# Kernel tuning notes

Hardware: AMD Instinct MI355X
Metric: run time of the kernel (lower is better)

The kernel has to match this reference:

```python
import jax, jax.numpy as jnp
import numpy as np

B, T, N, C, H = 8, 96, 1024, 64, 64  # batch, in_len, nodes, hidden_dim, MLP hidden
NUM_TYPES, EMB = 3, 8
GROUPS = 4


def setup_inputs() -> dict:
    key = jax.random.key(0)
    ks = jax.random.split(key, 16)
    s = 0.05
    return {
        "x": jax.random.normal(ks[0], (B, T, 1, N), jnp.float32),
        "adj": jax.random.uniform(ks[1], (N, N), jnp.float32) / N,  # row-normalized-ish
        "node_type": jax.random.randint(ks[2], (N,), 0, NUM_TYPES),
        # input_projection: Conv1d(1, C, 1) -> per-channel scale + bias
        "w_in": jax.random.normal(ks[3], (C,), jnp.float32) * np.sqrt(2.0),
        "b_in": jnp.zeros((C,), jnp.float32),
        # GCN params
        "weights_pool": jax.random.normal(ks[4], (EMB, C, C), jnp.float32) * np.sqrt(2.0 / (EMB + C)),
        "node_emb": jax.random.normal(ks[5], (NUM_TYPES, EMB), jnp.float32) * s,
        # GroupNorm(4, C)
        "gn_w": jnp.ones((C,), jnp.float32),
        "gn_b": jnp.zeros((C,), jnp.float32),
        # ResBlock temporal MLP: Linear(T,H) then Linear(H,T)
        "w1": jax.random.normal(ks[6], (H, T), jnp.float32) * np.sqrt(1.0 / T),
        "b1": jnp.zeros((H,), jnp.float32),
        "w2": jax.random.normal(ks[7], (T, H), jnp.float32) * np.sqrt(1.0 / H),
        "b2": jnp.zeros((T,), jnp.float32),
        # out_projection: Conv1d(C, 1, 1)
        "w_out": jax.random.normal(ks[8], (C,), jnp.float32) * np.sqrt(2.0 / C),
        "b_out": jnp.zeros((), jnp.float32),
    }


def reference(x, adj, node_type, w_in, b_in, weights_pool, node_emb,
              gn_w, gn_b, w1, b1, w2, b2, w_out, b_out):
    Bx, Tx, _, Nx = x.shape
    BT = Bx * Tx
    # input_projection: Conv1d(1->C, k=1) on (BT, 1, N)
    h = x.reshape(BT, Nx)                                   # channel dim is 1
    h = h[:, None, :] * w_in[None, :, None] + b_in[None, :, None]   # (BT, C, N)
    x_in = h
    # --- GCN with adaptive per-node weights ---
    feats = jnp.swapaxes(h, 1, 2)                            # (BT, N, C)
    nt_emb = node_emb[node_type]                             # gather -> (N, 8)
    node_w = jnp.einsum('nd,dio->nio', nt_emb, weights_pool) # (N, C, C)
    feats = jnp.einsum('nm,bmi->bni', adj, feats)            # adj @ feats
    feats = jnp.einsum('bni,nio->bno', feats, node_w)        # per-node matmul
    h = jnp.swapaxes(feats, 1, 2) + x_in                     # (BT, C, N)
    # --- GroupNorm(4, C), eps=1e-5 ---
    g = h.reshape(BT, GROUPS, C // GROUPS, Nx)
    mu = g.mean(axis=(2, 3), keepdims=True)
    var = g.var(axis=(2, 3), keepdims=True)
    g = (g - mu) / jnp.sqrt(var + 1e-5)
    h = g.reshape(BT, C, Nx) * gn_w[None, :, None] + gn_b[None, :, None]
    # --- temporal mixer: (b t) c n -> (b n) t c ---
    h = h.reshape(Bx, Tx, C, Nx).transpose(0, 3, 1, 2).reshape(Bx * Nx, Tx, C)
    ht = jnp.swapaxes(h, 1, 2)                               # (BN, C, T)
    t = jax.nn.relu(ht @ w1.T + b1) @ w2.T + b2              # (BN, C, T)
    h = h + jnp.swapaxes(t, 1, 2)                            # (BN, T, C)
    # --- silu + out_projection: Conv1d(C->1, k=1) over (BN, C, T) ---
    y = jax.nn.silu(jnp.swapaxes(h, 1, 2))                   # (BN, C, T)
    y = jnp.einsum('bct,c->bt', y, w_out) + b_out            # (BN, T)
    y = y.reshape(Bx, Nx, Tx).transpose(0, 2, 1)[:, :, None, :]  # (B, T, 1, N)
    return y
```

## Files before the change

### kernel.cpp

```cpp
#include <hip/hip_runtime.h>
#include <hip/hip_bf16.h>
#include <math.h>

#define B_   8
#define T_   96
#define N_   1024
#define C_   64
#define H_   64
#define BT_  768
#define EMB_ 8

typedef __attribute__((ext_vector_type(8))) short short8v;
typedef __attribute__((ext_vector_type(4))) float f32x4;

__device__ __forceinline__ ushort f2bf(float f) {
    unsigned int u = __float_as_uint(f);
    unsigned int r = (u + 0x7fffu + ((u >> 16) & 1u)) >> 16;
    return (ushort)r;
}
__device__ __forceinline__ float bf2f(ushort h) {
    return __uint_as_float(((unsigned int)h) << 16);
}

__global__ __launch_bounds__(256) void k_setup(const float* __restrict__ wpool,
                                               const float* __restrict__ w_in,
                                               const float* __restrict__ b_in,
                                               const float* __restrict__ emb,
                                               const float* __restrict__ w1,
                                               const float* __restrict__ w2,
                                               const float* __restrict__ x,
                                               ushort* __restrict__ wfrag1,
                                               ushort* __restrict__ wfrag2,
                                               float* __restrict__ xT,
                                               float* __restrict__ WT,
                                               float* __restrict__ BTb,
                                               float* __restrict__ TAB,
                                               float* __restrict__ GG) {
    int bid = blockIdx.x;
    int tid = threadIdx.x;
    if (bid == 0) {
        for (int e = tid; e < 6144; e += 256) {
            int j = e & 7, lane = (e >> 3) & 63, frag = e >> 9;
            int mt = frag / 3, k0 = frag - 3 * mt;
            int h = 16 * mt + (lane & 15);
            int t = 32 * k0 + 8 * (lane >> 4) + j;
            wfrag1[e] = f2bf(w1[h * T_ + t]);
        }
    } else if (bid == 1) {
        for (int e = tid; e < 6144; e += 256) {
            int j = e & 7, lane = (e >> 3) & 63, frag = e >> 9;
            int mt2 = frag >> 1, ks = frag & 1;
            int t = 16 * mt2 + (lane & 15);
            int h = 32 * ks + 8 * (lane >> 4) + j;
            wfrag2[e] = f2bf(w2[t * H_ + h]);
        }
    } else if (bid < 194) {
        __shared__ float tile[64][65];
        int tnum = bid - 2;
        int ti = tnum >> 4;
        int tj = tnum & 15;
#pragma unroll
        for (int k = 0; k < 16; ++k) {
            int idx = tid + 256 * k;
            int r = idx >> 6, cq = idx & 63;
            tile[r][cq] = x[(ti * 64 + r) * N_ + tj * 64 + cq];
        }
        __syncthreads();
#pragma unroll
        for (int k = 0; k < 16; ++k) {
            int idx = tid + 256 * k;
            int r = idx >> 6, cq = idx & 63;
            xT[(tj * 64 + r) * BT_ + ti * 64 + cq] = tile[cq][r];
        }
    } else {
        __shared__ float wp1s[512], wpbs[512];
        for (int e = tid; e < 512; e += 256) {
            int d = e >> 6, cc = e & 63;
            float s1 = 0.f, s2 = 0.f;
            for (int i = 0; i < 64; ++i) {
                float w = wpool[(d * 64 + i) * 64 + cc];
                s1 += w_in[i] * w;
                s2 += b_in[i] * w;
            }
            wp1s[e] = s1;
            wpbs[e] = s2;
        }
        __syncthreads();
        int wave = tid >> 6, lane = tid & 63;
        int lq = lane & 15, g = lane >> 4;
        if (wave < 3) {
            int ty = wave, cc = lane;
            float w = 0.f, bb = 0.f;
#pragma unroll
            for (int d = 0; d < EMB_; ++d) {
                float ev = emb[ty * EMB_ + d];
                w += ev * wp1s[d * C_ + cc];
                bb += ev * wpbs[d * C_ + cc];
            }
            WT[ty * C_ + cc] = w;
            BTb[ty * C_ + cc] = bb;
            float wi = w_in[cc], bi = b_in[cc];
            float vals[9] = {w, bb, w * w, bb * bb, w * wi, w * bi, wi * bb, bb * bi, w * bb};
#pragma unroll
            for (int q = 0; q < 9; ++q) {
                vals[q] += __shfl_xor(vals[q], 1);
                vals[q] += __shfl_xor(vals[q], 2);
                vals[q] += __shfl_xor(vals[q], 4);
                vals[q] += __shfl_xor(vals[q], 8);
            }
            if (lq == 0) {
#pragma unroll
                for (int q = 0; q < 9; ++q) TAB[(ty * 4 + g) * 9 + q] = vals[q];
            }
        } else {
            int cc = lane;
            float wi = w_in[cc], bi = b_in[cc];
            float v5[5] = {wi, bi, wi * wi, bi * bi, wi * bi};
#pragma unroll
            for (int q = 0; q < 5; ++q) {
                v5[q] += __shfl_xor(v5[q], 1);
                v5[q] += __shfl_xor(v5[q], 2);
                v5[q] += __shfl_xor(v5[q], 4);
                v5[q] += __shfl_xor(v5[q], 8);
            }
            if (lq == 0) {
#pragma unroll
                for (int q = 0; q < 5; ++q) GG[g * 5 + q] = v5[q];
            }
        }
    }
}

__global__ __launch_bounds__(256, 4) void k_ax(const float* __restrict__ x,
                                               const float* __restrict__ adj,
                                               float* __restrict__ axo,
                                               float* __restrict__ axT,
                                               float* __restrict__ rs) {
    __shared__ ushort Xs[32 * 64];
    __shared__ ushort As[32 * 64];
    const int tid = threadIdx.x;
    const int wave = tid >> 6, lane = tid & 63;
    const int lq = lane & 15, g4 = lane >> 4;
    const int n0 = blockIdx.x * 32, m0 = blockIdx.y * 32;
    const int mi = wave >> 1, ni = wave & 1;
    const int sr = tid >> 3, sq = tid & 7;
    const int sqx = sq ^ (sr & 7);
    const int ra = 16 * mi + lq, rb = 16 * ni + lq;

    f32x4 acc = {0.f, 0.f, 0.f, 0.f};
    float rsacc = 0.f;

    for (int k0 = 0; k0 < N_; k0 += 64) {
        __syncthreads();
        {
            const float* px = x + (m0 + sr) * N_ + k0 + sq * 8;
            float4 xa = *(const float4*)px;
            float4 xb = *(const float4*)(px + 4);
            union { short8v v; __hip_bfloat162 h[4]; } o;
            o.h[0] = __float22bfloat162_rn(make_float2(xa.x, xa.y));
            o.h[1] = __float22bfloat162_rn(make_float2(xa.z, xa.w));
            o.h[2] = __float22bfloat162_rn(make_float2(xb.x, xb.y));
            o.h[3] = __float22bfloat162_rn(make_float2(xb.z, xb.w));
            *(short8v*)&Xs[sr * 64 + sqx * 8] = o.v;

            const float* pa = adj + (n0 + sr) * N_ + k0 + sq * 8;
            float4 aa = *(const float4*)pa;
            float4 ab = *(const float4*)(pa + 4);
            if (m0 == 0)
                rsacc += aa.x + aa.y + aa.z + aa.w + ab.x + ab.y + ab.z + ab.w;
            o.h[0] = __float22bfloat162_rn(make_float2(aa.x, aa.y));
            o.h[1] = __float22bfloat162_rn(make_float2(aa.z, aa.w));
            o.h[2] = __float22bfloat162_rn(make_float2(ab.x, ab.y));
            o.h[3] = __float22bfloat162_rn(make_float2(ab.z, ab.w));
            *(short8v*)&As[sr * 64 + sqx * 8] = o.v;
        }
        __syncthreads();
#pragma unroll
        for (int ks = 0; ks < 2; ++ks) {
            short8v a = *(const short8v*)&Xs[ra * 64 + ((4 * ks + g4) ^ (ra & 7)) * 8];
            short8v bb = *(const short8v*)&As[rb * 64 + ((4 * ks + g4) ^ (rb & 7)) * 8];
            acc = __builtin_amdgcn_mfma_f32_16x16x32_bf16(a, bb, acc, 0, 0, 0);
        }
    }
    if (m0 == 0) {
        rsacc += __shfl_xor(rsacc, 1);
        rsacc += __shfl_xor(rsacc, 2);
        rsacc += __shfl_xor(rsacc, 4);
        if (sq == 0) rs[n0 + sr] = rsacc;
    }
#pragma unroll
    for (int r = 0; r < 4; ++r)
        axo[(m0 + 16 * mi + 4 * g4 + r) * N_ + n0 + 16 * ni + lq] = acc[r];
    float4 tv = make_float4(acc[0], acc[1], acc[2], acc[3]);
    *(float4*)&axT[(n0 + 16 * ni + lq) * BT_ + m0 + 16 * mi + 4 * g4] = tv;
}

__global__ __launch_bounds__(256) void k_gn(const float* __restrict__ x,
                                            const float* __restrict__ ax,
                                            const float* __restrict__ rs,
                                            const int* __restrict__ ntype,
                                            const float* __restrict__ TAB,
                                            const float* __restrict__ GG,
                                            float* __restrict__ muT,
                                            float* __restrict__ rgT) {
    int bt = blockIdx.x;
    int tid = threadIdx.x;
    const float* axr = ax + bt * N_;
    const float* xr = x + bt * N_;
    float S[23];
#pragma unroll
    for (int q = 0; q < 23; ++q) S[q] = 0.f;
#pragma unroll
    for (int i = 0; i < 4; ++i) {
        int n = tid + 256 * i;
        float a = axr[n], xv = xr[n], r = rs[n];
        int ty = ntype[n];
        float e0 = (ty == 0) ? 1.f : 0.f;
        float e1 = (ty == 1) ? 1.f : 0.f;
        float e2 = (ty == 2) ? 1.f : 0.f;
        float a2 = a * a, axp = a * xv, ar = a * r, xrr = xv * r, r2 = r * r;
        S[0] += e0 * a;   S[1] += e1 * a;   S[2] += e2 * a;
        S[3] += e0 * r;   S[4] += e1 * r;   S[5] += e2 * r;
        S[6] += e0 * a2;  S[7] += e1 * a2;  S[8] += e2 * a2;
        S[9] += e0 * r2;  S[10] += e1 * r2; S[11] += e2 * r2;
        S[12] += e0 * axp; S[13] += e1 * axp; S[14] += e2 * axp;
        S[15] += e0 * ar; S[16] += e1 * ar; S[17] += e2 * ar;
        S[18] += e0 * xrr; S[19] += e1 * xrr; S[20] += e2 * xrr;
        S[21] += xv;      S[22] += xv * xv;
    }
#pragma unroll
    for (int q = 0; q < 23; ++q) {
#pragma unroll
        for (int off = 32; off; off >>= 1) S[q] += __shfl_down(S[q], off);
    }
    __shared__ float wred[4][23];
    __shared__ float tot[23];
    int wave = tid >> 6, lane = tid & 63;
    if (lane == 0) {
#pragma unroll
        for (int q = 0; q < 23; ++q) wred[wave][q] = S[q];
    }
    __syncthreads();
    if (tid < 23) tot[tid] = wred[0][tid] + wred[1][tid] + wred[2][tid] + wred[3][tid];
    __syncthreads();
    if (tid < 4) {
        int g = tid;
        float M = 0.f, Q = 0.f;
#pragma unroll
        for (int ty = 0; ty < 3; ++ty) {
            const float* tb = TAB + (ty * 4 + g) * 9;
            float A1v = tot[0 + ty], R1v = tot[3 + ty], A2v = tot[6 + ty];
            float R2v = tot[9 + ty], AXv = tot[12 + ty], ARv = tot[15 + ty];
            float XRv = tot[18 + ty];
            M += tb[0] * A1v + tb[1] * R1v;
            Q += tb[2] * A2v + tb[3] * R2v +
                 2.f * (tb[4] * AXv + tb[5] * A1v + tb[6] * XRv + tb[7] * R1v + tb[8] * ARv);
        }
        float Sx = tot[21], Sx2 = tot[22];
        const float* gg = GG + g * 5;
        M += gg[0] * Sx + 1024.f * gg[1];
        Q += gg[2] * Sx2 + 2.f * gg[4] * Sx + 1024.f * gg[3];
        const float inv = 1.f / 16384.f;
        float m = M * inv;
        float v = Q * inv - m * m;
        int b = bt / T_, t = bt - b * T_;
        muT[(b * 4 + g) * T_ + t] = m;
        rgT[(b * 4 + g) * T_ + t] = rsqrtf(v + 1e-5f);
    }
}

__global__ __launch_bounds__(256, 4) void k_main(const float* __restrict__ xT,
                                                 const float* __restrict__ axT,
                                                 const float* __restrict__ rs,
                                                 const int* __restrict__ ntype,
                                                 const float* __restrict__ WT,
                                                 const float* __restrict__ BTb,
                                                 const float* __restrict__ muT,
                                                 const float* __restrict__ rgT,
                                                 const float* __restrict__ w_in,
                                                 const float* __restrict__ b_in,
                                                 const float* __restrict__ gn_w,
                                                 const float* __restrict__ gn_b,
                                                 const ushort* __restrict__ wfrag1,
                                                 const ushort* __restrict__ wfrag2,
                                                 const float* __restrict__ b1,
                                                 const float* __restrict__ b2,
                                                 const float* __restrict__ w_out,
                                                 const float* __restrict__ b_out,
                                                 float* __restrict__ out) {
    __shared__ ushort Hs[64 * 104];
    __shared__ ushort Hd[64 * 104];
    __shared__ float axs[4][96], xs[4][96];
    __shared__ float musT[4 * 100], rgsT[4 * 100];
    __shared__ float redp[4][96][4];

    const int tid = threadIdx.x;
    const int n0 = blockIdx.x * 4;
    const int b = blockIdx.y;
    const int wm = tid >> 6;
    const int lane = tid & 63;
    const int lq = lane & 15;
    const int g4 = lane >> 4;

    short8v w1f[4][3];
#pragma unroll
    for (int mt = 0; mt < 4; ++mt)
#pragma unroll
        for (int k0 = 0; k0 < 3; ++k0)
            w1f[mt][k0] = *(const short8v*)(wfrag1 + (((mt * 3 + k0) << 6) + lane) * 8);

    for (int j = tid; j < 384; j += 256) {
        int nn = j / 96, t = j - nn * 96;
        axs[nn][t] = axT[(n0 + nn) * BT_ + b * T_ + t];
        xs[nn][t] = xT[(n0 + nn) * BT_ + b * T_ + t];
    }
    for (int j = tid; j < 384; j += 256) {
        int g = j / 96, t = j - 96 * g;
        musT[g * 100 + t] = muT[b * 384 + j];
        rgsT[g * 100 + t] = rgT[b * 384 + j];
    }

    const int c = 16 * wm + lq;
    const float wic = w_in[c], bic = b_in[c];
    const float gwc = gn_w[c], gbc = gn_b[c];

    const int4 ty4 = *(const int4*)&ntype[n0];
    const float4 rs4 = *(const float4*)&rs[n0];
    float wlc4[4], base4[4];
    {
        const float wlcA[3] = {WT[c], WT[64 + c], WT[128 + c]};
        const float blcA[3] = {BTb[c], BTb[64 + c], BTb[128 + c]};
        const int tys[4] = {ty4.x, ty4.y, ty4.z, ty4.w};
        const float rss[4] = {rs4.x, rs4.y, rs4.z, rs4.w};
#pragma unroll
        for (int nn = 0; nn < 4; ++nn) {
            int ty = tys[nn];
            float wlc = (ty == 0) ? wlcA[0] : (ty == 1) ? wlcA[1] : wlcA[2];
            float blc = (ty == 0) ? blcA[0] : (ty == 1) ? blcA[1] : blcA[2];
            wlc4[nn] = wlc;
            base4[nn] = rss[nn] * blc + bic;
        }
    }
    __syncthreads();

    const ushort* wf2p = wfrag2;
    const float* b1p = b1;
    const float* b2p = b2;
    const float* wop = w_out;

#pragma unroll 1
    for (int nn = 0; nn < 4; ++nn) {
        asm volatile("" : "+s"(wf2p), "+s"(b1p), "+s"(b2p), "+s"(wop));
        const float wlc = wlc4[nn];
        const float base = base4[nn];

        f32x4 acc1[4] = {{0.f, 0.f, 0.f, 0.f}, {0.f, 0.f, 0.f, 0.f},
                         {0.f, 0.f, 0.f, 0.f}, {0.f, 0.f, 0.f, 0.f}};
#pragma unroll
        for (int k0 = 0; k0 < 3; ++k0) {
            int t8 = 32 * k0 + 8 * g4;
            float4 a0 = *(const float4*)&axs[nn][t8];
            float4 a1 = *(const float4*)&axs[nn][t8 + 4];
            float4 x0 = *(const float4*)&xs[nn][t8];
            float4 x1 = *(const float4*)&xs[nn][t8 + 4];
            float4 m0 = *(const float4*)&musT[wm * 100 + t8];
            float4 m1 = *(const float4*)&musT[wm * 100 + t8 + 4];
            float4 r0 = *(const float4*)&rgsT[wm * 100 + t8];
            float4 r1 = *(const float4*)&rgsT[wm * 100 + t8 + 4];
            float vv[8];
            vv[0] = ((a0.x * wlc + x0.x * wic + base) - m0.x) * (r0.x * gwc) + gbc;
            vv[1] = ((a0.y * wlc + x0.y * wic + base) - m0.y) * (r0.y * gwc) + gbc;
            vv[2] = ((a0.z * wlc + x0.z * wic + base) - m0.z) * (r0.z * gwc) + gbc;
            vv[3] = ((a0.w * wlc + x0.w * wic + base) - m0.w) * (r0.w * gwc) + gbc;
            vv[4] = ((a1.x * wlc + x1.x * wic + base) - m1.x) * (r1.x * gwc) + gbc;
            vv[5] = ((a1.y * wlc + x1.y * wic + base) - m1.y) * (r1.y * gwc) + gbc;
            vv[6] = ((a1.z * wlc + x1.z * wic + base) - m1.z) * (r1.z * gwc) + gbc;
            vv[7] = ((a1.w * wlc + x1.w * wic + base) - m1.w) * (r1.w * gwc) + gbc;
            union { short8v v; __hip_bfloat162 h2[4]; } o;
            o.h2[0] = __float22bfloat162_rn(make_float2(vv[0], vv[1]));
            o.h2[1] = __float22bfloat162_rn(make_float2(vv[2], vv[3]));
            o.h2[2] = __float22bfloat162_rn(make_float2(vv[4], vv[5]));
            o.h2[3] = __float22bfloat162_rn(make_float2(vv[6], vv[7]));
            *(short8v*)&Hs[c * 104 + t8] = o.v;
#pragma unroll
            for (int mt = 0; mt < 4; ++mt)
                acc1[mt] = __builtin_amdgcn_mfma_f32_16x16x32_bf16(w1f[mt][k0], o.v, acc1[mt], 0, 0, 0);
        }

#pragma unroll
        for (int mt = 0; mt < 4; ++mt) {
            float4 b1v = *(const float4*)(b1p + 16 * mt + 4 * g4);
            __hip_bfloat162 p0 = __float22bfloat162_rn(make_float2(
                fmaxf(acc1[mt][0] + b1v.x, 0.f), fmaxf(acc1[mt][1] + b1v.y, 0.f)));
            __hip_bfloat162 p1 = __float22bfloat162_rn(make_float2(
                fmaxf(acc1[mt][2] + b1v.z, 0.f), fmaxf(acc1[mt][3] + b1v.w, 0.f)));
            union { uint2 u; __hip_bfloat162 h2[2]; } w;
            w.h2[0] = p0; w.h2[1] = p1;
            *(uint2*)&Hd[c * 104 + 16 * mt + 4 * g4] = w.u;
        }

        f32x4 acc2[6] = {{0.f, 0.f, 0.f, 0.f}, {0.f, 0.f, 0.f, 0.f},
                         {0.f, 0.f, 0.f, 0.f}, {0.f, 0.f, 0.f, 0.f},
                         {0.f, 0.f, 0.f, 0.f}, {0.f, 0.f, 0.f, 0.f}};
#pragma unroll
        for (int ks = 0; ks < 2; ++ks) {
            short8v af = *(const short8v*)&Hd[c * 104 + 32 * ks + 8 * g4];
#pragma unroll
            for (int mt2 = 0; mt2 < 6; ++mt2) {
                short8v bf = *(const short8v*)(wf2p + (((mt2 * 2 + ks) << 6) + lane) * 8);
                acc2[mt2] = __builtin_amdgcn_mfma_f32_16x16x32_bf16(af, bf, acc2[mt2], 0, 0, 0);
            }
        }

        float4 wo4 = *(const float4*)(wop + 16 * wm + 4 * g4);
#pragma unroll
        for (int mt2 = 0; mt2 < 6; ++mt2) {
            int tv = 16 * mt2 + lq;
            float bz = b2p[tv];
            float pm = 0.f;
#pragma unroll
            for (int r = 0; r < 4; ++r) {
                float res = bf2f(Hs[(16 * wm + 4 * g4 + r) * 104 + tv]);
                float z = res + acc2[mt2][r] + bz;
                float sg = __builtin_amdgcn_rcpf(1.f + __expf(-z));
                pm += z * sg * wo4[r];
            }
            pm += __shfl_xor(pm, 16);
            pm += __shfl_xor(pm, 32);
            if (g4 == 0) redp[nn][tv][wm] = pm;
        }
    }
    __syncthreads();

    if (tid < 96) {
        float bo = b_out[0];
        float4 y;
        float* py = (float*)&y;
#pragma unroll
        for (int nn = 0; nn < 4; ++nn) {
            float4 v = *(const float4*)&redp[nn][tid][0];
            py[nn] = v.x + v.y + v.z + v.w + bo;
        }
        *(float4*)&out[(b * T_ + tid) * N_ + n0] = y;
    }
}

extern "C" void kernel_launch(void* const* d_in, const int* in_sizes, int n_in,
                              void* d_out, int out_size, void* d_ws, size_t ws_size,
                              hipStream_t stream) {
    const float* x     = (const float*)d_in[0];
    const float* adj   = (const float*)d_in[1];
    const int*   ntype = (const int*)d_in[2];
    const float* w_in  = (const float*)d_in[3];
    const float* b_in  = (const float*)d_in[4];
    const float* wpool = (const float*)d_in[5];
    const float* emb   = (const float*)d_in[6];
    const float* gn_w  = (const float*)d_in[7];
    const float* gn_b  = (const float*)d_in[8];
    const float* w1    = (const float*)d_in[9];
    const float* b1    = (const float*)d_in[10];
    const float* w2    = (const float*)d_in[11];
    const float* b2    = (const float*)d_in[12];
    const float* w_out = (const float*)d_in[13];
    const float* b_out = (const float*)d_in[14];
    float* out = (float*)d_out;
    float* ws = (float*)d_ws;

    float* rsv  = ws + 1024;
    float* WT   = ws + 2048;
    float* BTb  = ws + 2240;
    float* TAB  = ws + 2432;
    float* GG   = ws + 2540;
    float* muT  = ws + 2560;
    float* rgT  = ws + 5632;
    ushort* wfrag1 = (ushort*)(ws + 8704);
    ushort* wfrag2 = (ushort*)(ws + 11776);
    float* axb  = ws + 14848;
    float* axTb = ws + 14848 + 786432;
    float* xTb  = ws + 14848 + 2 * 786432;

    k_setup<<<dim3(195), dim3(256), 0, stream>>>(wpool, w_in, b_in, emb, w1, w2, x,
                                                 wfrag1, wfrag2, xTb, WT, BTb, TAB, GG);
    k_ax<<<dim3(32, 24), dim3(256), 0, stream>>>(x, adj, axb, axTb, rsv);
    k_gn<<<dim3(768), dim3(256), 0, stream>>>(x, axb, rsv, ntype, TAB, GG, muT, rgT);
    k_main<<<dim3(256, 8), dim3(256), 0, stream>>>(xTb, axTb, rsv, ntype, WT, BTb,
                                                   muT, rgT, w_in, b_in, gn_w, gn_b,
                                                   wfrag1, wfrag2, b1, b2,
                                                   w_out, b_out, out);
}
```

Before: 83.21 us.

## Merge setup and adj-matmul kernels; precompute GroupNorm affine in registers in main

The setup kernel and the adj@x MFMA kernel are merged into one launch with a block-id dispatch and a shared-memory union. This removes one kernel launch and lets the two independent workloads run concurrently. In k_main, the shared-memory staging of mu and rstd is replaced by per-thread register loads folded with gn_w and gn_b into FMA form. The w1 fragments are now reloaded from global memory inside the loop instead of held in registers, trading register pressure for extra loads.

Result: no change. 83.47 us (+0.3%).

```diff
diff --git a/kernel.cpp b/kernel.cpp
--- a/kernel.cpp
+++ b/kernel.cpp
@@ -22,23 +22,88 @@
     return __uint_as_float(((unsigned int)h) << 16);
 }
 
-__global__ __launch_bounds__(256) void k_setup(const float* __restrict__ wpool,
-                                               const float* __restrict__ w_in,
-                                               const float* __restrict__ b_in,
-                                               const float* __restrict__ emb,
-                                               const float* __restrict__ w1,
-                                               const float* __restrict__ w2,
-                                               const float* __restrict__ x,
-                                               ushort* __restrict__ wfrag1,
-                                               ushort* __restrict__ wfrag2,
-                                               float* __restrict__ xT,
-                                               float* __restrict__ WT,
-                                               float* __restrict__ BTb,
-                                               float* __restrict__ TAB,
-                                               float* __restrict__ GG) {
-    int bid = blockIdx.x;
-    int tid = threadIdx.x;
-    if (bid == 0) {
+__global__ __launch_bounds__(256, 4) void k_pre(const float* __restrict__ x,
+                                                const float* __restrict__ adj,
+                                                const float* __restrict__ wpool,
+                                                const float* __restrict__ w_in,
+                                                const float* __restrict__ b_in,
+                                                const float* __restrict__ emb,
+                                                const float* __restrict__ w1,
+                                                const float* __restrict__ w2,
+                                                float* __restrict__ axo,
+                                                float* __restrict__ axT,
+                                                float* __restrict__ rs,
+                                                ushort* __restrict__ wfrag1,
+                                                ushort* __restrict__ wfrag2,
+                                                float* __restrict__ xT,
+                                                float* __restrict__ WT,
+                                                float* __restrict__ BTb,
+                                                float* __restrict__ TAB,
+                                                float* __restrict__ GG) {
+    __shared__ union UU {
+        struct { ushort Xs[32 * 64]; ushort As[32 * 64]; } g;
+        float tile[64][65];
+        struct { float wp1s[512]; float wpbs[512]; } tab;
+    } U;
+    const int bid = blockIdx.x;
+    const int tid = threadIdx.x;
+
+    if (bid < 768) {
+        const int wave = tid >> 6, lane = tid & 63;
+        const int lq = lane & 15, g4 = lane >> 4;
+        const int n0 = (bid & 31) * 32, m0 = (bid >> 5) * 32;
+        const int mi = wave >> 1, ni = wave & 1;
+        const int sr = tid >> 3, sq = tid & 7;
+        const int sqx = sq ^ (sr & 7);
+        const int ra = 16 * mi + lq, rb = 16 * ni + lq;
+
+        f32x4 acc = {0.f, 0.f, 0.f, 0.f};
+        float rsacc = 0.f;
+
+        for (int k0 = 0; k0 < N_; k0 += 64) {
+            __syncthreads();
+            {
+                const float* px = x + (m0 + sr) * N_ + k0 + sq * 8;
+                float4 xa = *(const float4*)px;
+                float4 xb = *(const float4*)(px + 4);
+                union { short8v v; __hip_bfloat162 h[4]; } o;
+                o.h[0] = __float22bfloat162_rn(make_float2(xa.x, xa.y));
+                o.h[1] = __float22bfloat162_rn(make_float2(xa.z, xa.w));
+                o.h[2] = __float22bfloat162_rn(make_float2(xb.x, xb.y));
+                o.h[3] = __float22bfloat162_rn(make_float2(xb.z, xb.w));
+                *(short8v*)&U.g.Xs[sr * 64 + sqx * 8] = o.v;
+
+                const float* pa = adj + (n0 + sr) * N_ + k0 + sq * 8;
+                float4 aa = *(const float4*)pa;
+                float4 ab = *(const float4*)(pa + 4);
+                if (m0 == 0)
+                    rsacc += aa.x + aa.y + aa.z + aa.w + ab.x + ab.y + ab.z + ab.w;
+                o.h[0] = __float22bfloat162_rn(make_float2(aa.x, aa.y));
+                o.h[1] = __float22bfloat162_rn(make_float2(aa.z, aa.w));
+                o.h[2] = __float22bfloat162_rn(make_float2(ab.x, ab.y));
+                o.h[3] = __float22bfloat162_rn(make_float2(ab.z, ab.w));
+                *(short8v*)&U.g.As[sr * 64 + sqx * 8] = o.v;
+            }
+            __syncthreads();
+#pragma unroll
+            for (int ks = 0; ks < 2; ++ks) {
+                short8v a = *(const short8v*)&U.g.Xs[ra * 64 + ((4 * ks + g4) ^ (ra & 7)) * 8];
+                short8v bb = *(const short8v*)&U.g.As[rb * 64 + ((4 * ks + g4) ^ (rb & 7)) * 8];
+                acc = __builtin_amdgcn_mfma_f32_16x16x32_bf16(a, bb, acc, 0, 0, 0);
+            }
+        }
+        if (m0 == 0) {
+            rsacc += __shfl_xor(rsacc, 1);
+            rsacc += __shfl_xor(rsacc, 2);
+            rsacc += __shfl_xor(rsacc, 4);
+            if (sq == 0) rs[n0 + sr] = rsacc;
+        }
+#pragma unroll
+        for (int r = 0; r < 4; ++r)
+            axo[(m0 + 16 * mi + 4 * g4 + r) * N_ + n0 + 16 * ni + lq] = acc[r];
+        float4 tv = make_float4(acc[0], acc[1], acc[2], acc[3]);
+        *(float4*)&axT[(n0 + 16 * ni + lq) * BT_ + m0 + 16 * mi + 4 * g4] = tv;
+    } else if (bid == 768) {
         for (int e = tid; e < 6144; e += 256) {
             int j = e & 7, lane = (e >> 3) & 63, frag = e >> 9;
             int mt = frag / 3, k0 = frag - 3 * mt;
@@ -46,7 +111,7 @@
             int t = 32 * k0 + 8 * (lane >> 4) + j;
             wfrag1[e] = f2bf(w1[h * T_ + t]);
         }
-    } else if (bid == 1) {
+    } else if (bid == 769) {
         for (int e = tid; e < 6144; e += 256) {
             int j = e & 7, lane = (e >> 3) & 63, frag = e >> 9;
             int mt2 = frag >> 1, ks = frag & 1;
@@ -54,26 +119,24 @@
             int h = 32 * ks + 8 * (lane >> 4) + j;
             wfrag2[e] = f2bf(w2[t * H_ + h]);
         }
-    } else if (bid < 194) {
-        __shared__ float tile[64][65];
-        int tnum = bid - 2;
+    } else if (bid < 962) {
+        int tnum = bid - 770;
         int ti = tnum >> 4;
         int tj = tnum & 15;
 #pragma unroll
         for (int k = 0; k < 16; ++k) {
             int idx = tid + 256 * k;
             int r = idx >> 6, cq = idx & 63;
-            tile[r][cq] = x[(ti * 64 + r) * N_ + tj * 64 + cq];
+            U.tile[r][cq] = x[(ti * 64 + r) * N_ + tj * 64 + cq];
         }
         __syncthreads();
 #pragma unroll
         for (int k = 0; k < 16; ++k) {
             int idx = tid + 256 * k;
             int r = idx >> 6, cq = idx & 63;
-            xT[(tj * 64 + r) * BT_ + ti * 64 + cq] = tile[cq][r];
+            xT[(tj * 64 + r) * BT_ + ti * 64 + cq] = U.tile[cq][r];
         }
     } else {
-        __shared__ float wp1s[512], wpbs[512];
         for (int e = tid; e < 512; e += 256) {
             int d = e >> 6, cc = e & 63;
             float s1 = 0.f, s2 = 0.f;
@@ -82,8 +145,8 @@
                 s1 += w_in[i] * w;
                 s2 += b_in[i] * w;
             }
-            wp1s[e] = s1;
-            wpbs[e] = s2;
+            U.tab.wp1s[e] = s1;
+            U.tab.wpbs[e] = s2;
         }
         __syncthreads();
         int wave = tid >> 6, lane = tid & 63;
@@ -94,8 +157,8 @@
 #pragma unroll
             for (int d = 0; d < EMB_; ++d) {
                 float ev = emb[ty * EMB_ + d];
-                w += ev * wp1s[d * C_ + cc];
-                bb += ev * wpbs[d * C_ + cc];
+                w += ev * U.tab.wp1s[d * C_ + cc];
+                bb += ev * U.tab.wpbs[d * C_ + cc];
             }
             WT[ty * C_ + cc] = w;
             BTb[ty * C_ + cc] = bb;
@@ -129,70 +192,6 @@
             }
         }
     }
-}
-
-__global__ __launch_bounds__(256, 4) void k_ax(const float* __restrict__ x,
-                                               const float* __restrict__ adj,
-                                               float* __restrict__ axo,
-                                               float* __restrict__ axT,
-                                               float* __restrict__ rs) {
-    __shared__ ushort Xs[32 * 64];
-    __shared__ ushort As[32 * 64];
-    const int tid = threadIdx.x;
-    const int wave = tid >> 6, lane = tid & 63;
-    const int lq = lane & 15, g4 = lane >> 4;
-    const int n0 = blockIdx.x * 32, m0 = blockIdx.y * 32;
-    const int mi = wave >> 1, ni = wave & 1;
-    const int sr = tid >> 3, sq = tid & 7;
-    const int sqx = sq ^ (sr & 7);
-    const int ra = 16 * mi + lq, rb = 16 * ni + lq;
-
-    f32x4 acc = {0.f, 0.f, 0.f, 0.f};
-    float rsacc = 0.f;
-
-    for (int k0 = 0; k0 < N_; k0 += 64) {
-        __syncthreads();
-        {
-            const float* px = x + (m0 + sr) * N_ + k0 + sq * 8;
-            float4 xa = *(const float4*)px;
-            float4 xb = *(const float4*)(px + 4);
-            union { short8v v; __hip_bfloat162 h[4]; } o;
-            o.h[0] = __float22bfloat162_rn(make_float2(xa.x, xa.y));
-            o.h[1] = __float22bfloat162_rn(make_float2(xa.z, xa.w));
-            o.h[2] = __float22bfloat162_rn(make_float2(xb.x, xb.y));
-            o.h[3] = __float22bfloat162_rn(make_float2(xb.z, xb.w));
-            *(short8v*)&Xs[sr * 64 + sqx * 8] = o.v;
-
-            const float* pa = adj + (n0 + sr) * N_ + k0 + sq * 8;
-            float4 aa = *(const float4*)pa;
-            float4 ab = *(const float4*)(pa + 4);
-            if (m0 == 0)
-                rsacc += aa.x + aa.y + aa.z + aa.w + ab.x + ab.y + ab.z + ab.w;
-            o.h[0] = __float22bfloat162_rn(make_float2(aa.x, aa.y));
-            o.h[1] = __float22bfloat162_rn(make_float2(aa.z, aa.w));
-            o.h[2] = __float22bfloat162_rn(make_float2(ab.x, ab.y));
-            o.h[3] = __float22bfloat162_rn(make_float2(ab.z, ab.w));
-            *(short8v*)&As[sr * 64 + sqx * 8] = o.v;
-        }
-        __syncthreads();
-#pragma unroll
-        for (int ks = 0; ks < 2; ++ks) {
-            short8v a = *(const short8v*)&Xs[ra * 64 + ((4 * ks + g4) ^ (ra & 7)) * 8];
-            short8v bb = *(const short8v*)&As[rb * 64 + ((4 * ks + g4) ^ (rb & 7)) * 8];
-            acc = __builtin_amdgcn_mfma_f32_16x16x32_bf16(a, bb, acc, 0, 0, 0);
-        }
-    }
-    if (m0 == 0) {
-        rsacc += __shfl_xor(rsacc, 1);
-        rsacc += __shfl_xor(rsacc, 2);
-        rsacc += __shfl_xor(rsacc, 4);
-        if (sq == 0) rs[n0 + sr] = rsacc;
-    }
-#pragma unroll
-    for (int r = 0; r < 4; ++r)
-        axo[(m0 + 16 * mi + 4 * g4 + r) * N_ + n0 + 16 * ni + lq] = acc[r];
-    float4 tv = make_float4(acc[0], acc[1], acc[2], acc[3]);
-    *(float4*)&axT[(n0 + 16 * ni + lq) * BT_ + m0 + 16 * mi + 4 * g4] = tv;
 }
 
 __global__ __launch_bounds__(256) void k_gn(const float* __restrict__ x,
@@ -291,7 +290,6 @@
     __shared__ ushort Hs[64 * 104];
     __shared__ ushort Hd[64 * 104];
     __shared__ float axs[4][96], xs[4][96];
-    __shared__ float musT[4 * 100], rgsT[4 * 100];
     __shared__ float redp[4][96][4];
 
     const int tid = threadIdx.x;
@@ -302,47 +300,37 @@
     const int lq = lane & 15;
     const int g4 = lane >> 4;
 
-    short8v w1f[4][3];
-#pragma unroll
-    for (int mt = 0; mt < 4; ++mt)
-#pragma unroll
-        for (int k0 = 0; k0 < 3; ++k0)
-            w1f[mt][k0] = *(const short8v*)(wfrag1 + (((mt * 3 + k0) << 6) + lane) * 8);
-
     for (int j = tid; j < 384; j += 256) {
         int nn = j / 96, t = j - nn * 96;
         axs[nn][t] = axT[(n0 + nn) * BT_ + b * T_ + t];
         xs[nn][t] = xT[(n0 + nn) * BT_ + b * T_ + t];
     }
-    for (int j = tid; j < 384; j += 256) {
-        int g = j / 96, t = j - 96 * g;
-        musT[g * 100 + t] = muT[b * 384 + j];
-        rgsT[g * 100 + t] = rgT[b * 384 + j];
-    }
 
     const int c = 16 * wm + lq;
     const float wic = w_in[c], bic = b_in[c];
     const float gwc = gn_w[c], gbc = gn_b[c];
-
-    const int4 ty4 = *(const int4*)&ntype[n0];
-    const float4 rs4 = *(const float4*)&rs[n0];
-    float wlc4[4], base4[4];
-    {
-        const float wlcA[3] = {WT[c], WT[64 + c], WT[128 + c]};
-        const float blcA[3] = {BTb[c], BTb[64 + c], BTb[128 + c]};
-        const int tys[4] = {ty4.x, ty4.y, ty4.z, ty4.w};
-        const float rss[4] = {rs4.x, rs4.y, rs4.z, rs4.w};
-#pragma unroll
-        for (int nn = 0; nn < 4; ++nn) {
-            int ty = tys[nn];
-            float wlc = (ty == 0) ? wlcA[0] : (ty == 1) ? wlcA[1] : wlcA[2];
-            float blc = (ty == 0) ? blcA[0] : (ty == 1) ? blcA[1] : blcA[2];
-            wlc4[nn] = wlc;
-            base4[nn] = rss[nn] * blc + bic;
-        }
+    const float wlcA[3] = {WT[c], WT[64 + c], WT[128 + c]};
+    const float blcA[3] = {BTb[c], BTb[64 + c], BTb[128 + c]};
+
+    float4 rgA[3], rgB[3], mgA[3], mgB[3];
+#pragma unroll
+    for (int k0 = 0; k0 < 3; ++k0) {
+        const float* mp = muT + b * 384 + wm * 96 + 32 * k0 + 8 * g4;
+        const float* rp = rgT + b * 384 + wm * 96 + 32 * k0 + 8 * g4;
+        float4 mA = *(const float4*)mp;
+        float4 mB = *(const float4*)(mp + 4);
+        float4 rA = *(const float4*)rp;
+        float4 rB = *(const float4*)(rp + 4);
+        rgA[k0] = make_float4(rA.x * gwc, rA.y * gwc, rA.z * gwc, rA.w * gwc);
+        rgB[k0] = make_float4(rB.x * gwc, rB.y * gwc, rB.z * gwc, rB.w * gwc);
+        mgA[k0] = make_float4(gbc - mA.x * rgA[k0].x, gbc - mA.y * rgA[k0].y,
+                              gbc - mA.z * rgA[k0].z, gbc - mA.w * rgA[k0].w);
+        mgB[k0] = make_float4(gbc - mB.x * rgB[k0].x, gbc - mB.y * rgB[k0].y,
+                              gbc - mB.z * rgB[k0].z, gbc - mB.w * rgB[k0].w);
     }
     __syncthreads();
 
+    const ushort* wf1p = wfrag1;
     const ushort* wf2p = wfrag2;
     const float* b1p = b1;
     const float* b2p = b2;
@@ -350,9 +338,12 @@
 
 #pragma unroll 1
     for (int nn = 0; nn < 4; ++nn) {
-        asm volatile("" : "+s"(wf2p), "+s"(b1p), "+s"(b2p), "+s"(wop));
-        const float wlc = wlc4[nn];
-        const float base = base4[nn];
+        asm volatile("" : "+s"(wf1p), "+s"(wf2p), "+s"(b1p), "+s"(b2p), "+s"(wop));
+        const int n = n0 + nn;
+        const int ty = ntype[n];
+        const float wlc = (ty == 0) ? wlcA[0] : (ty == 1) ? wlcA[1] : wlcA[2];
+        const float blc = (ty == 0) ? blcA[0] : (ty == 1) ? blcA[1] : blcA[2];
+        const float base = fmaf(rs[n], blc, bic);
 
         f32x4 acc1[4] = {{0.f, 0.f, 0.f, 0.f}, {0.f, 0.f, 0.f, 0.f},
                          {0.f, 0.f, 0.f, 0.f}, {0.f, 0.f, 0.f, 0.f}};
@@ -363,19 +354,15 @@
             float4 a1 = *(const float4*)&axs[nn][t8 + 4];
             float4 x0 = *(const float4*)&xs[nn][t8];
             float4 x1 = *(const float4*)&xs[nn][t8 + 4];
-            float4 m0 = *(const float4*)&musT[wm * 100 + t8];
-            float4 m1 = *(const float4*)&musT[wm * 100 + t8 + 4];
-            float4 r0 = *(const float4*)&rgsT[wm * 100 + t8];
-            float4 r1 = *(const float4*)&rgsT[wm * 100 + t8 + 4];
             float vv[8];
-            vv[0] = ((a0.x * wlc + x0.x * wic + base) - m0.x) * (r0.x * gwc) + gbc;
-            vv[1] = ((a0.y * wlc + x0.y * wic + base) - m0.y) * (r0.y * gwc) + gbc;
-            vv[2] = ((a0.z * wlc + x0.z * wic + base) - m0.z) * (r0.z * gwc) + gbc;
-            vv[3] = ((a0.w * wlc + x0.w * wic + base) - m0.w) * (r0.w * gwc) + gbc;
-            vv[4] = ((a1.x * wlc + x1.x * wic + base) - m1.x) * (r1.x * gwc) + gbc;
-            vv[5] = ((a1.y * wlc + x1.y * wic + base) - m1.y) * (r1.y * gwc) + gbc;
-            vv[6] = ((a1.z * wlc + x1.z * wic + base) - m1.z) * (r1.z * gwc) + gbc;
-            vv[7] = ((a1.w * wlc + x1.w * wic + base) - m1.w) * (r1.w * gwc) + gbc;
+            vv[0] = fmaf(fmaf(a0.x, wlc, fmaf(x0.x, wic, base)), rgA[k0].x, mgA[k0].x);
+            vv[1] = fmaf(fmaf(a0.y, wlc, fmaf(x0.y, wic, base)), rgA[k0].y, mgA[k0].y);
+            vv[2] = fmaf(fmaf(a0.z, wlc, fmaf(x0.z, wic, base)), rgA[k0].z, mgA[k0].z);
+            vv[3] = fmaf(fmaf(a0.w, wlc, fmaf(x0.w, wic, base)), rgA[k0].w, mgA[k0].w);
+            vv[4] = fmaf(fmaf(a1.x, wlc, fmaf(x1.x, wic, base)), rgB[k0].x, mgB[k0].x);
+            vv[5] = fmaf(fmaf(a1.y, wlc, fmaf(x1.y, wic, base)), rgB[k0].y, mgB[k0].y);
+            vv[6] = fmaf(fmaf(a1.z, wlc, fmaf(x1.z, wic, base)), rgB[k0].z, mgB[k0].z);
+            vv[7] = fmaf(fmaf(a1.w, wlc, fmaf(x1.w, wic, base)), rgB[k0].w, mgB[k0].w);
             union { short8v v; __hip_bfloat162 h2[4]; } o;
             o.h2[0] = __float22bfloat162_rn(make_float2(vv[0], vv[1]));
             o.h2[1] = __float22bfloat162_rn(make_float2(vv[2], vv[3]));
@@ -383,8 +370,10 @@
             o.h2[3] = __float22bfloat162_rn(make_float2(vv[6], vv[7]));
             *(short8v*)&Hs[c * 104 + t8] = o.v;
 #pragma unroll
-            for (int mt = 0; mt < 4; ++mt)
-                acc1[mt] = __builtin_amdgcn_mfma_f32_16x16x32_bf16(w1f[mt][k0], o.v, acc1[mt], 0, 0, 0);
+            for (int mt = 0; mt < 4; ++mt) {
+                short8v wv = *(const short8v*)(wf1p + (((mt * 3 + k0) << 6) + lane) * 8);
+                acc1[mt] = __builtin_amdgcn_mfma_f32_16x16x32_bf16(wv, o.v, acc1[mt], 0, 0, 0);
+            }
         }
 
 #pragma unroll
@@ -479,9 +468,9 @@
     float* axTb = ws + 14848 + 786432;
     float* xTb  = ws + 14848 + 2 * 786432;
 
-    k_setup<<<dim3(195), dim3(256), 0, stream>>>(wpool, w_in, b_in, emb, w1, w2, x,
-                                                 wfrag1, wfrag2, xTb, WT, BTb, TAB, GG);
-    k_ax<<<dim3(32, 24), dim3(256), 0, stream>>>(x, adj, axb, axTb, rsv);
+    k_pre<<<dim3(963), dim3(256), 0, stream>>>(x, adj, wpool, w_in, b_in, emb, w1, w2,
+                                               axb, axTb, rsv, wfrag1, wfrag2, xTb,
+                                               WT, BTb, TAB, GG);
     k_gn<<<dim3(768), dim3(256), 0, stream>>>(x, axb, rsv, ntype, TAB, GG, muT, rgT);
     k_main<<<dim3(256, 8), dim3(256), 0, stream>>>(xTb, axTb, rsv, ntype, WT, BTb,
                                                    muT, rgT, w_in, b_in, gn_w, gn_b,
```
